# Kernel tuning notes

Hardware: AMD Instinct MI355X
Metric: run time of the kernel (lower is better)

## Reference

```python
import jax, jax.numpy as jnp
import numpy as np

D_MODEL = 1024
N_HEADS = 16
HEAD_DIM = D_MODEL // N_HEADS
D_FF = 4096
ROPE_BASE = 10000.0
LN_EPS = 1e-5


def setup_inputs() -> dict:
    key = jax.random.key(0)
    ks = jax.random.split(key, 12)
    B, S = 2, 2048
    s = 0.02
    inp = {
        "x": jax.random.normal(ks[0], (B, S, D_MODEL), dtype=jnp.float32),
        "Wq": jax.random.normal(ks[1], (D_MODEL, D_MODEL), dtype=jnp.float32) * s,
        "bq": jnp.zeros((D_MODEL,), jnp.float32),
        "Wk": jax.random.normal(ks[2], (D_MODEL, D_MODEL), dtype=jnp.float32) * s,
        "bk": jnp.zeros((D_MODEL,), jnp.float32),
        "Wv": jax.random.normal(ks[3], (D_MODEL, D_MODEL), dtype=jnp.float32) * s,
        "bv": jnp.zeros((D_MODEL,), jnp.float32),
        "Wo": jax.random.normal(ks[4], (D_MODEL, D_MODEL), dtype=jnp.float32) * s,
        "bo": jnp.zeros((D_MODEL,), jnp.float32),
        "ln1_g": jnp.ones((D_MODEL,), jnp.float32),
        "ln1_b": jnp.zeros((D_MODEL,), jnp.float32),
        "W1": jax.random.normal(ks[5], (D_MODEL, D_FF), dtype=jnp.float32) * s,
        "b1": jnp.zeros((D_FF,), jnp.float32),
        "W2": jax.random.normal(ks[6], (D_FF, D_MODEL), dtype=jnp.float32) * s,
        "b2": jnp.zeros((D_MODEL,), jnp.float32),
        "ln2_g": jnp.ones((D_MODEL,), jnp.float32),
        "ln2_b": jnp.zeros((D_MODEL,), jnp.float32),
    }
    return inp


def _layernorm(x, g, b):
    mu = jnp.mean(x, axis=-1, keepdims=True)
    var = jnp.var(x, axis=-1, keepdims=True)
    return (x - mu) * jax.lax.rsqrt(var + LN_EPS) * g + b


def _rope_cos_sin(seq_len, dtype):
    inv_freq = 1.0 / (ROPE_BASE ** (jnp.arange(0, HEAD_DIM, 2, dtype=jnp.float32) / HEAD_DIM))
    t = jnp.arange(seq_len, dtype=jnp.float32)
    freqs = jnp.einsum("i,j->ij", t, inv_freq)          # [S, HEAD_DIM/2]
    emb = jnp.concatenate([freqs, freqs], axis=-1)        # [S, HEAD_DIM]
    return jnp.cos(emb).astype(dtype), jnp.sin(emb).astype(dtype)


def _rotate_half(x):
    x1, x2 = jnp.split(x, 2, axis=-1)
    return jnp.concatenate([-x2, x1], axis=-1)


def reference(x, Wq, bq, Wk, bk, Wv, bv, Wo, bo, ln1_g, ln1_b,
              W1, b1, W2, b2, ln2_g, ln2_b):
    B, S, _ = x.shape
    residual = x
    h = _layernorm(x, ln1_g, ln1_b)

    def split_heads(y):  # [B,S,D] -> [B,H,S,hd]
        return y.reshape(B, S, N_HEADS, HEAD_DIM).transpose(0, 2, 1, 3)

    q = split_heads(h @ Wq + bq)
    k = split_heads(h @ Wk + bk)
    v = split_heads(h @ Wv + bv)

    cos, sin = _rope_cos_sin(S, x.dtype)  # [S, hd], broadcast over B,H
    q = q * cos + _rotate_half(q) * sin
    k = k * cos + _rotate_half(k) * sin

    scale = HEAD_DIM ** -0.5
    scores = jnp.einsum("bhqd,bhkd->bhqk", q, k) * scale
    attn = jax.nn.softmax(scores, axis=-1)
    ctx = jnp.einsum("bhqk,bhkd->bhqd", attn, v)           # [B,H,S,hd]
    ctx = ctx.transpose(0, 2, 1, 3).reshape(B, S, D_MODEL)
    attn_out = ctx @ Wo + bo

    x = residual + attn_out
    residual = x
    h = _layernorm(x, ln2_g, ln2_b)
    ffn = jax.nn.gelu(h @ W1 + b1, approximate=False) @ W2 + b2
    return residual + ffn
```

## Files before the change

kernel.cpp:

```cpp
#include <hip/hip_runtime.h>
#include <hip/hip_bf16.h>
#include <stdint.h>

#define S_LEN 2048
#define NH 16
#define HD 64
#define DM 1024
#define DFF 4096
#define MTOK 4096

typedef __attribute__((ext_vector_type(8))) short short8;
typedef __attribute__((ext_vector_type(4))) float f32x4;
typedef __attribute__((ext_vector_type(16))) float f32x16;
typedef __attribute__((ext_vector_type(2))) int i32x2;
typedef unsigned short u16;
typedef unsigned int u32;

__device__ __forceinline__ float bf2f(u16 u) {
  union { u32 i; float f; } x; x.i = ((u32)u) << 16; return x.f;
}
__device__ __forceinline__ u16 f2bf(float f) {
  union { float f; u32 i; } x; x.f = f;
  u32 r = x.i + 0x7fffu + ((x.i >> 16) & 1u);
  return (u16)(r >> 16);
}
__device__ __forceinline__ float exp2_fast(float x) {
  union { int i; float f; } u;
  u.i = (int)__builtin_fmaf(x, 8388608.0f, 1064986823.0f);
  return u.f;
}
__device__ __forceinline__ void gload16(const u16* g, u16* l) {
  __builtin_amdgcn_global_load_lds(
      (__attribute__((address_space(1))) u32*)g,
      (__attribute__((address_space(3))) u32*)l, 16, 0, 0);
}

#define VM0 asm volatile("s_waitcnt vmcnt(0)" ::: "memory")
#define VM6 asm volatile("s_waitcnt vmcnt(6)" ::: "memory")
#define BARR do { __builtin_amdgcn_s_barrier(); asm volatile("" ::: "memory"); } while (0)
#define LGKM0 do { asm volatile("s_waitcnt lgkmcnt(0)" ::: "memory"); __builtin_amdgcn_sched_barrier(0); } while (0)
#define PRIO1 __builtin_amdgcn_s_setprio(1)
#define PRIO0 __builtin_amdgcn_s_setprio(0)

__device__ __forceinline__ void transpose_tile(const float* __restrict__ W,
                                               u16* __restrict__ Wt, int K, int N,
                                               int n0, int k0, int tx, int ty,
                                               float (*tile)[33]) {
#pragma unroll
  for (int i = 0; i < 4; ++i)
    tile[ty + i * 8][tx] = W[(size_t)(k0 + ty + i * 8) * N + n0 + tx];
  __syncthreads();
#pragma unroll
  for (int i = 0; i < 4; ++i)
    Wt[(size_t)(n0 + ty + i * 8) * K + k0 + tx] = f2bf(tile[tx][ty + i * 8]);
}

__global__ __launch_bounds__(256) void prep(
    const float* __restrict__ Wq, const float* __restrict__ Wk,
    const float* __restrict__ Wv, const float* __restrict__ Wo,
    const float* __restrict__ W1, const float* __restrict__ W2,
    u16* __restrict__ WQKVT, u16* __restrict__ WOT, u16* __restrict__ W1T,
    u16* __restrict__ W2T, float* __restrict__ cosT, float* __restrict__ sinT,
    const float* __restrict__ x, const float* __restrict__ g,
    const float* __restrict__ b, u16* __restrict__ H) {
  __shared__ float tile[32][33];
  __shared__ float red[8];
  const int r = blockIdx.x;
  const int t = threadIdx.x;
  const int tx = t & 31, ty = t >> 5;
  if (r < 4096) {
    const float* W = (r < 1024) ? Wq : (r < 2048) ? Wk : (r < 3072) ? Wv : Wo;
    u16* Wt = (r < 1024) ? WQKVT
              : (r < 2048) ? WQKVT + 1024 * 1024
              : (r < 3072) ? WQKVT + 2 * 1024 * 1024 : WOT;
    int sub = r & 1023;
    transpose_tile(W, Wt, 1024, 1024, (sub & 31) * 32, (sub >> 5) * 32, tx, ty, tile);
  } else if (r < 8192) {
    int sub = r - 4096;
    transpose_tile(W1, W1T, 1024, 4096, (sub & 127) * 32, (sub >> 7) * 32, tx, ty, tile);
  } else if (r < 12288) {
    int sub = r - 8192;
    transpose_tile(W2, W2T, 4096, 1024, (sub & 31) * 32, (sub >> 5) * 32, tx, ty, tile);
  } else if (r < 12544) {
    int id = (r - 12288) * 256 + t;
    int s = id >> 5, j = id & 31;
    float inv = powf(10000.0f, -(float)j * (1.0f / 32.0f));
    float fr = (float)s * inv;
    cosT[id] = cosf(fr);
    sinT[id] = sinf(fr);
  } else {
    int row = r - 12544;
    float4 v = ((const float4*)(x + ((size_t)row << 10)))[t];
    float s = v.x + v.y + v.z + v.w;
    float q = v.x * v.x + v.y * v.y + v.z * v.z + v.w * v.w;
#pragma unroll
    for (int m = 1; m < 64; m <<= 1) {
      s += __shfl_xor(s, m, 64);
      q += __shfl_xor(q, m, 64);
    }
    int lane = t & 63, w = t >> 6;
    if (lane == 0) { red[w] = s; red[4 + w] = q; }
    __syncthreads();
    s = red[0] + red[1] + red[2] + red[3];
    q = red[4] + red[5] + red[6] + red[7];
    float mu = s * (1.0f / 1024.0f);
    float var = q * (1.0f / 1024.0f) - mu * mu;
    float rstd = rsqrtf(var + 1e-5f);
    float4 gv = ((const float4*)g)[t];
    float4 bv = ((const float4*)b)[t];
    ushort4 o;
    o.x = f2bf((v.x - mu) * rstd * gv.x + bv.x);
    o.y = f2bf((v.y - mu) * rstd * gv.y + bv.y);
    o.z = f2bf((v.z - mu) * rstd * gv.z + bv.z);
    o.w = f2bf((v.w - mu) * rstd * gv.w + bv.w);
    ((ushort4*)(H + ((size_t)row << 10)))[t] = o;
  }
}

__global__ __launch_bounds__(256) void ln_bf16(const float* __restrict__ x,
                                               const float* __restrict__ g,
                                               const float* __restrict__ b,
                                               u16* __restrict__ out) {
  int row = blockIdx.x;
  int t = threadIdx.x;
  float4 v = ((const float4*)(x + ((size_t)row << 10)))[t];
  float s = v.x + v.y + v.z + v.w;
  float q = v.x * v.x + v.y * v.y + v.z * v.z + v.w * v.w;
#pragma unroll
  for (int m = 1; m < 64; m <<= 1) {
    s += __shfl_xor(s, m, 64);
    q += __shfl_xor(q, m, 64);
  }
  __shared__ float red[8];
  int lane = t & 63, w = t >> 6;
  if (lane == 0) { red[w] = s; red[4 + w] = q; }
  __syncthreads();
  s = red[0] + red[1] + red[2] + red[3];
  q = red[4] + red[5] + red[6] + red[7];
  float mu = s * (1.0f / 1024.0f);
  float var = q * (1.0f / 1024.0f) - mu * mu;
  float rstd = rsqrtf(var + 1e-5f);
  float4 gv = ((const float4*)g)[t];
  float4 bv = ((const float4*)b)[t];
  ushort4 o;
  o.x = f2bf((v.x - mu) * rstd * gv.x + bv.x);
  o.y = f2bf((v.y - mu) * rstd * gv.y + bv.y);
  o.z = f2bf((v.z - mu) * rstd * gv.z + bv.z);
  o.w = f2bf((v.w - mu) * rstd * gv.w + bv.w);
  ((ushort4*)(out + ((size_t)row << 10)))[t] = o;
}

#define MMQ4(IB, NB)                                                         \
  _Pragma("unroll") for (int i_ = 0; i_ < 4; ++i_)                           \
  _Pragma("unroll") for (int n_ = 0; n_ < 2; ++n_)                           \
  _Pragma("unroll") for (int k_ = 0; k_ < 2; ++k_)                           \
    acc[(IB) + i_][(NB) + n_] = __builtin_amdgcn_mfma_f32_16x16x32_bf16(     \
        a[(IB) + i_][k_], b[(NB) + n_][k_], acc[(IB) + i_][(NB) + n_], 0, 0, 0);

template <int EPI>
__global__ __launch_bounds__(512, 1) void gemm256(
    const u16* __restrict__ A, const u16* __restrict__ Bt, int N, int K,
    const float* __restrict__ bias, const float* __restrict__ bq,
    const float* __restrict__ bk, const float* __restrict__ bv,
    const float* __restrict__ cosT, const float* __restrict__ sinT,
    u16* __restrict__ d0, u16* __restrict__ d1, u16* __restrict__ d2) {
  __shared__ __align__(16) u16 As[2][256 * 64];
  __shared__ __align__(16) u16 Bs[2][256 * 64];
  const int t = threadIdx.x;
  const int lane = t & 63, wid = t >> 6;
  const int fr = lane & 15, fq = lane >> 4;
  const int m0 = blockIdx.y << 8, n0 = blockIdx.x << 8;
  const int wmo = (wid >> 2) << 7;
  const int wno = (wid & 3) << 6;
  const int r7 = fr & 7;
  const int ssl = t & 7;
  const u16* Ap = A + (size_t)m0 * K;
  const u16* Bp = Bt + (size_t)n0 * K;

  f32x4 acc[8][4];
#pragma unroll
  for (int i = 0; i < 8; ++i)
#pragma unroll
    for (int n = 0; n < 4; ++n) acc[i][n] = (f32x4){0.f, 0.f, 0.f, 0.f};

  short8 a[8][2], b[4][2];

  auto stageH = [&](u16* dstSlot, const u16* src, int rowOff, int kt) {
#pragma unroll
    for (int c = 0; c < 2; ++c) {
      const int R = rowOff + (c << 6) + (t >> 3);
      gload16(src + (size_t)R * K + kt + ((ssl ^ (R & 7)) << 3),
              dstSlot + (size_t)R * 64 + ssl * 8);
    }
  };
  auto readAall = [&](int slot) {
#pragma unroll
    for (int i = 0; i < 8; ++i) {
      const u16* rp = &As[slot][(wmo + (i << 4) + fr) << 6];
      a[i][0] = *(const short8*)(rp + ((fq ^ r7) << 3));
      a[i][1] = *(const short8*)(rp + (((4 + fq) ^ r7) << 3));
    }
  };
  auto readB2 = [&](int slot, int nbase) {
#pragma unroll
    for (int n = 0; n < 2; ++n) {
      const u16* rp = &Bs[slot][(wno + ((nbase + n) << 4) + fr) << 6];
      b[nbase + n][0] = *(const short8*)(rp + ((fq ^ r7) << 3));
      b[nbase + n][1] = *(const short8*)(rp + (((4 + fq) ^ r7) << 3));
    }
  };

  const int nt = K >> 6;
  stageH(&As[0][0], Ap, 0, 0);
  stageH(&As[0][0], Ap, 128, 0);
  stageH(&Bs[0][0], Bp, 0, 0);
  stageH(&Bs[0][0], Bp, 128, 0);
  stageH(&As[1][0], Ap, 0, 64);
  stageH(&As[1][0], Ap, 128, 64);
  stageH(&Bs[1][0], Bp, 0, 64);

  for (int tt = 0; tt < nt; ++tt) {
    const int s = tt & 1;
    const int kt1 = (tt + 1) << 6, kt2 = (tt + 2) << 6;
    if (tt + 1 < nt) { VM6; } else { VM0; }
    BARR;
    readAall(s);
    readB2(s, 0);
    if (tt + 1 < nt) stageH(&Bs[s ^ 1][0], Bp, 128, kt1);
    LGKM0;
    PRIO1; MMQ4(0, 0); PRIO0;
    BARR;
    readB2(s, 2);
    if (tt + 2 < nt) stageH(&As[s][0], Ap, 0, kt2);
    LGKM0;
    PRIO1; MMQ4(0, 2); PRIO0;
    BARR;
    if (tt + 2 < nt) stageH(&As[s][0], Ap, 128, kt2);
    PRIO1; MMQ4(4, 2); PRIO0;
    BARR;
    if (tt + 2 < nt) stageH(&Bs[s][0], Bp, 0, kt2);
    PRIO1; MMQ4(4, 0); PRIO0;
  }

  if (EPI == 0) {
    const int colbase = n0 + wno;
    const int slice = colbase >> 10;
    const int cb = colbase & 1023;
    const int hh = cb >> 6;
    if (slice < 2) {
      const float sc = (slice == 0) ? 0.125f * 1.44269504088896f : 1.0f;
      const float* bb_ = (slice == 0) ? bq : bk;
      u16* dst = (slice == 0) ? d0 : d1;
#pragma unroll
      for (int i = 0; i < 8; ++i) {
        const int row0 = m0 + wmo + (i << 4) + (fq << 2);
#pragma unroll
        for (int n = 0; n < 2; ++n) {
          const int d = n * 16 + fr;
          const float blo = bb_[cb + d];
          const float bhi = bb_[cb + d + 32];
#pragma unroll
          for (int j = 0; j < 4; ++j) {
            const int row = row0 + j;
            const int ss = row & 2047, bb2 = row >> 11;
            const float c = cosT[ss * 32 + d];
            const float sn = sinT[ss * 32 + d];
            const float av = acc[i][n][j] + blo;
            const float bv2 = acc[i][n + 2][j] + bhi;
            const size_t base = ((size_t)((bb2 * 16 + hh) * 2048 + ss)) << 6;
            dst[base + d] = f2bf((av * c - bv2 * sn) * sc);
            dst[base + d + 32] = f2bf((bv2 * c + av * sn) * sc);
          }
        }
      }
    } else {
#pragma unroll
      for (int i = 0; i < 8; ++i) {
        const int row0 = m0 + wmo + (i << 4) + (fq << 2);
#pragma unroll
        for (int n = 0; n < 4; ++n) {
          const int d = n * 16 + fr;
          const float bia = bv[cb + d];
#pragma unroll
          for (int j = 0; j < 4; ++j) {
            const int row = row0 + j;
            const int ss = row & 2047, bb2 = row >> 11;
            d2[((size_t)((bb2 * 16 + hh) * 64 + d)) * 2048 + ss] =
                f2bf(acc[i][n][j] + bia);
          }
        }
      }
    }
  } else {
#pragma unroll
    for (int i = 0; i < 8; ++i) {
      const int row0 = m0 + wmo + (i << 4) + (fq << 2);
#pragma unroll
      for (int n = 0; n < 4; ++n) {
        const int col = n0 + wno + n * 16 + fr;
        const float bia = bias[col];
#pragma unroll
        for (int j = 0; j < 4; ++j) {
          const int row = row0 + j;
          const float v = acc[i][n][j] + bia;
          const float gl = 0.5f * v * (1.0f + erff(v * 0.70710678118f));
          d0[(size_t)row * N + col] = f2bf(gl);
        }
      }
    }
  }
}

__global__ __launch_bounds__(512, 1) void gemm_split(
    const u16* __restrict__ A, const u16* __restrict__ Bt, int K,
    const float* __restrict__ bias, const float* __restrict__ resid,
    float* __restrict__ dst) {
  __shared__ __align__(16) u16 As[2][128 * 128];
  __shared__ __align__(16) u16 Bs[2][128 * 128];
  const int t = threadIdx.x, lane = t & 63, w = t >> 6;
  const int fr = lane & 15, fq = lane >> 4;
  const int wq = w & 3, kh = w >> 2;
  const int wm = (wq >> 1) << 6, wn = (wq & 1) << 6;
  const int bid = blockIdx.x;
  const int xcd = bid & 7, within = bid >> 3;
  const int m0 = (xcd * 4 + (within >> 3)) << 7;
  const int n0 = (within & 7) << 7;
  const int srow = t >> 4;
  const int ssl = t & 15;

  f32x4 acc[4][4];
#pragma unroll
  for (int i = 0; i < 4; ++i)
#pragma unroll
    for (int n = 0; n < 4; ++n) acc[i][n] = (f32x4){0.f, 0.f, 0.f, 0.f};

  auto stage = [&](int buf, int kt) {
#pragma unroll
    for (int c = 0; c < 4; ++c) {
      const int R = c * 32 + srow;
      const int gs = ssl ^ (R & 15);
      gload16(A + (size_t)(m0 + R) * K + kt + gs * 8, &As[buf][R * 128 + ssl * 8]);
    }
#pragma unroll
    for (int c = 0; c < 4; ++c) {
      const int R = c * 32 + srow;
      const int gs = ssl ^ (R & 15);
      gload16(Bt + (size_t)(n0 + R) * K + kt + gs * 8, &Bs[buf][R * 128 + ssl * 8]);
    }
  };

  stage(0, 0);
  int buf = 0;
  const int iters = K >> 7;
  for (int it = 0; it < iters; ++it) {
    VM0;
    BARR;
    if (it + 1 < iters) stage(buf ^ 1, (it + 1) << 7);

    short8 a[4][2], b[4][2];
#pragma unroll
    for (int i = 0; i < 4; ++i) {
      const u16* rp = &As[buf][(wm + i * 16 + fr) * 128];
#pragma unroll
      for (int ks = 0; ks < 2; ++ks)
        a[i][ks] = *(const short8*)(rp + (((kh * 8 + ks * 4 + fq) ^ fr) << 3));
    }
#pragma unroll
    for (int n = 0; n < 4; ++n) {
      const u16* rp = &Bs[buf][(wn + n * 16 + fr) * 128];
#pragma unroll
      for (int ks = 0; ks < 2; ++ks)
        b[n][ks] = *(const short8*)(rp + (((kh * 8 + ks * 4 + fq) ^ fr) << 3));
    }
    PRIO1;
#pragma unroll
    for (int i = 0; i < 4; ++i)
#pragma unroll
      for (int n = 0; n < 4; ++n)
#pragma unroll
        for (int ks = 0; ks < 2; ++ks)
          acc[i][n] = __builtin_amdgcn_mfma_f32_16x16x32_bf16(a[i][ks], b[n][ks],
                                                              acc[i][n], 0, 0, 0);
    PRIO0;
    buf ^= 1;
  }

  BARR;
  float* mrg = (float*)&As[0][0];
  if (kh == 1) {
#pragma unroll
    for (int i = 0; i < 4; ++i) {
      const int ri = i * 16 + (fq << 2);
#pragma unroll
      for (int n = 0; n < 4; ++n) {
        const int ci = n * 16 + fr;
        *(f32x4*)(mrg + wq * 4352 + ci * 68 + ri) = acc[i][n];
      }
    }
  }
  LGKM0;
  BARR;
  if (kh == 0) {
#pragma unroll
    for (int i = 0; i < 4; ++i) {
      const int ri = i * 16 + (fq << 2);
      const int row0 = m0 + wm + ri;
#pragma unroll
      for (int n = 0; n < 4; ++n) {
        const int ci = n * 16 + fr;
        const int col = n0 + wn + ci;
        const f32x4 other = *(const f32x4*)(mrg + wq * 4352 + ci * 68 + ri);
        const float bia = bias[col];
#pragma unroll
        for (int j = 0; j < 4; ++j) {
          size_t idx = (size_t)(row0 + j) * 1024 + col;
          dst[idx] = acc[i][n][j] + other[j] + bia + resid[idx];
        }
      }
    }
  }
}

__global__ __launch_bounds__(512, 4) void attn_fwd(const u16* __restrict__ q,
                                                   const u16* __restrict__ k,
                                                   const u16* __restrict__ vt,
                                                   u16* __restrict__ ctx) {
  __shared__ __align__(16) u16 Ks[2][2][64 * 64];
  __shared__ __align__(16) u16 Vs[2][2][64 * 64];
  __shared__ float Lr[4][32];
  const int t = threadIdx.x, lane = t & 63, w = t >> 6;
  const int qsub = w & 3, half = w >> 2;
  const int ql = lane & 31;
  const int h = lane >> 5;
  const int bid = blockIdx.x;
  const int bh = (bid & 7) * 4 + ((bid >> 3) & 3);
  const int qt = bid >> 5;
  const int q0w = qt * 128 + qsub * 32;
  const size_t hbase = (size_t)bh << 17;
  const u16* kg = k + hbase;
  const u16* vg = vt + hbase;
  const int srow = t >> 3;
  const int sl = t & 7;
  const int l7 = lane & 7;

  short8 qf[4];
#pragma unroll
  for (int f = 0; f < 4; ++f)
    qf[f] = *(const short8*)(q + hbase + (size_t)(q0w + ql) * 64 + f * 16 + h * 8);

  float la[4] = {0.f, 0.f, 0.f, 0.f};
  f32x16 o[2];
#pragma unroll
  for (int db = 0; db < 2; ++db)
#pragma unroll
    for (int r = 0; r < 16; ++r) o[db][r] = 0.f;

  auto stage = [&](int buf, int it1) {
    const int kt0 = it1 << 6;
    const int kt1 = (16 + it1) << 6;
    const int gs = sl ^ (srow & 7);
    gload16(kg + (size_t)(kt0 + srow) * 64 + gs * 8, &Ks[0][buf][srow * 64 + sl * 8]);
    gload16(kg + (size_t)(kt1 + srow) * 64 + gs * 8, &Ks[1][buf][srow * 64 + sl * 8]);
    gload16(vg + (size_t)srow * 2048 + kt0 + gs * 8, &Vs[0][buf][srow * 64 + sl * 8]);
    gload16(vg + (size_t)srow * 2048 + kt1 + gs * 8, &Vs[1][buf][srow * 64 + sl * 8]);
  };

  stage(0, 0);
  int buf = 0;
  for (int it = 0; it < 16; ++it) {
    VM0;
    BARR;
    if (it < 15) stage(buf ^ 1, it + 1);

    f32x16 s[2];
    PRIO1;
#pragma unroll
    for (int kb = 0; kb < 2; ++kb) {
#pragma unroll
      for (int r = 0; r < 16; ++r) s[kb][r] = 0.f;
#pragma unroll
      for (int f = 0; f < 4; ++f) {
        const u16* kr = &Ks[half][buf][(kb * 32 + ql) * 64 + (((2 * f + h) ^ l7) << 3)];
        s[kb] = __builtin_amdgcn_mfma_f32_32x32x16_bf16(*(const short8*)kr, qf[f],
                                                        s[kb], 0, 0, 0);
      }
    }
    PRIO0;

    float p[2][16];
#pragma unroll
    for (int kb = 0; kb < 2; ++kb)
#pragma unroll
      for (int r = 0; r < 16; ++r) {
        p[kb][r] = exp2_fast(s[kb][r]);
        la[r & 3] += p[kb][r];
      }

    short8 pf[4];
#pragma unroll
    for (int kb = 0; kb < 2; ++kb)
#pragma unroll
      for (int rrp = 0; rrp < 2; ++rrp) {
        u32 y0, y1, x0, x1;
        asm volatile("v_cvt_pk_bf16_f32 %0, %1, %2" : "=v"(y0)
                     : "v"(p[kb][8 * rrp + 0]), "v"(p[kb][8 * rrp + 1]));
        asm volatile("v_cvt_pk_bf16_f32 %0, %1, %2" : "=v"(y1)
                     : "v"(p[kb][8 * rrp + 2]), "v"(p[kb][8 * rrp + 3]));
        asm volatile("v_cvt_pk_bf16_f32 %0, %1, %2" : "=v"(x0)
                     : "v"(p[kb][8 * rrp + 4]), "v"(p[kb][8 * rrp + 5]));
        asm volatile("v_cvt_pk_bf16_f32 %0, %1, %2" : "=v"(x1)
                     : "v"(p[kb][8 * rrp + 6]), "v"(p[kb][8 * rrp + 7]));
        i32x2 r0 = __builtin_amdgcn_permlane32_swap((int)x0, (int)y0, false, false);
        i32x2 r1 = __builtin_amdgcn_permlane32_swap((int)x1, (int)y1, false, false);
        u32 dw[4] = {(u32)r0[1], (u32)r1[1], (u32)r0[0], (u32)r1[0]};
        pf[kb * 2 + rrp] = *(short8*)dw;
      }

    PRIO1;
#pragma unroll
    for (int db = 0; db < 2; ++db) {
#pragma unroll
      for (int f = 0; f < 4; ++f) {
        const u16* vr = &Vs[half][buf][(db * 32 + ql) * 64 + (((2 * f + h) ^ l7) << 3)];
        o[db] = __builtin_amdgcn_mfma_f32_32x32x16_bf16(pf[f], *(const short8*)vr,
                                                        o[db], 0, 0, 0);
      }
    }
    PRIO0;
    buf ^= 1;
  }

  float lacc = (la[0] + la[1]) + (la[2] + la[3]);
  lacc += __shfl_xor(lacc, 32, 64);

  BARR;
  float* mO = (float*)&Ks[0][0][0];
  float* mL = (float*)&Vs[0][0][0];
  if (half == 1) {
#pragma unroll
    for (int r = 0; r < 16; ++r) {
      const int qr = (r & 3) + 8 * (r >> 2) + 4 * h;
#pragma unroll
      for (int db = 0; db < 2; ++db)
        mO[(qsub * 32 + qr) * 64 + db * 32 + ql] = o[db][r];
    }
    if (h == 0) mL[qsub * 32 + ql] = lacc;
  }
  LGKM0;
  BARR;
  if (half == 0) {
    float lsum = lacc + mL[qsub * 32 + ql];
    Lr[qsub][ql] = 1.0f / lsum;
#pragma unroll
    for (int r = 0; r < 16; ++r) {
      const int qr = (r & 3) + 8 * (r >> 2) + 4 * h;
#pragma unroll
      for (int db = 0; db < 2; ++db)
        o[db][r] += mO[(qsub * 32 + qr) * 64 + db * 32 + ql];
    }
    LGKM0;
    const int bb = bh >> 4, hh = bh & 15;
#pragma unroll
    for (int r = 0; r < 16; ++r) {
      const int qr = (r & 3) + 8 * (r >> 2) + 4 * h;
      const float rl = Lr[qsub][qr];
      const int row = q0w + qr;
      const size_t base = (((size_t)(bb * 2048 + row)) << 10) + hh * 64;
#pragma unroll
      for (int db = 0; db < 2; ++db)
        ctx[base + db * 32 + ql] = f2bf(o[db][r] * rl);
    }
  }
}

extern "C" void kernel_launch(void* const* d_in, const int* in_sizes, int n_in,
                              void* d_out, int out_size, void* d_ws, size_t ws_size,
                              hipStream_t stream) {
  const float* x    = (const float*)d_in[0];
  const float* Wq   = (const float*)d_in[1];
  const float* bq   = (const float*)d_in[2];
  const float* Wk   = (const float*)d_in[3];
  const float* bk   = (const float*)d_in[4];
  const float* Wv   = (const float*)d_in[5];
  const float* bv   = (const float*)d_in[6];
  const float* Wo   = (const float*)d_in[7];
  const float* bo   = (const float*)d_in[8];
  const float* ln1g = (const float*)d_in[9];
  const float* ln1b = (const float*)d_in[10];
  const float* W1   = (const float*)d_in[11];
  const float* b1   = (const float*)d_in[12];
  const float* W2   = (const float*)d_in[13];
  const float* b2   = (const float*)d_in[14];
  const float* ln2g = (const float*)d_in[15];
  const float* ln2b = (const float*)d_in[16];

  char* ws = (char*)d_ws;
  size_t off = 0;
  auto alloc = [&](size_t bytes) {
    char* p = ws + off;
    off += (bytes + 1023) & ~(size_t)1023;
    return p;
  };
  u16* WQKVT = (u16*)alloc((size_t)3 * DM * DM * 2);
  u16* WOT = (u16*)alloc((size_t)DM * DM * 2);
  u16* W1T = (u16*)alloc((size_t)DFF * DM * 2);
  u16* W2T = (u16*)alloc((size_t)DM * DFF * 2);
  float* COS = (float*)alloc((size_t)S_LEN * 32 * 4);
  float* SIN = (float*)alloc((size_t)S_LEN * 32 * 4);
  u16* H   = (u16*)alloc((size_t)MTOK * DM * 2);
  u16* Qb  = (u16*)alloc((size_t)MTOK * DM * 2);
  u16* Kb  = (u16*)alloc((size_t)MTOK * DM * 2);
  u16* VT  = (u16*)alloc((size_t)MTOK * DM * 2);
  u16* CTX = (u16*)alloc((size_t)MTOK * DM * 2);
  float* X2 = (float*)alloc((size_t)MTOK * DM * 4);
  u16* FFN1 = Qb;
  if (ws_size < off) return;

  dim3 blk256(256);
  prep<<<dim3(16640), blk256, 0, stream>>>(Wq, Wk, Wv, Wo, W1, W2, WQKVT, WOT,
                                           W1T, W2T, COS, SIN, x, ln1g, ln1b, H);
  gemm256<0><<<dim3(12, 16), dim3(512), 0, stream>>>(
      H, WQKVT, 3072, 1024, nullptr, bq, bk, bv, COS, SIN, Qb, Kb, VT);
  attn_fwd<<<dim3(512), dim3(512), 0, stream>>>(Qb, Kb, VT, CTX);
  gemm_split<<<dim3(256), dim3(512), 0, stream>>>(CTX, WOT, 1024, bo, x, X2);
  ln_bf16<<<4096, blk256, 0, stream>>>(X2, ln2g, ln2b, H);
  gemm256<1><<<dim3(16, 16), dim3(512), 0, stream>>>(
      H, W1T, 4096, 1024, b1, nullptr, nullptr, nullptr, nullptr, nullptr,
      FFN1, nullptr, nullptr);
  gemm_split<<<dim3(256), dim3(512), 0, stream>>>(FFN1, W2T, 4096, b2, X2, (float*)d_out);
}
```

Measured before the change: 220.2 us.

## Halve A-fragment registers and re-split GEMM staging into quarter-tile loads

The 256x256 GEMM mainloop now keeps only four A fragments in registers instead of eight, reading the two halves of the A tile in separate phases. Global-to-LDS staging is split into 64-row quarter loads that are reordered so each LDS region is refilled only after its last read. The vmcnt wait and barrier move to the end of each iteration. The aim is to cut VGPR pressure and spread loads more evenly, at the cost of extra barriers and LDS reads per k-step.

After: 223.6 us. Within noise of the previous version (+1.6%).

```diff
diff --git a/kernel.cpp b/kernel.cpp
--- a/kernel.cpp
+++ b/kernel.cpp
@@ -155,7 +155,7 @@
   _Pragma("unroll") for (int n_ = 0; n_ < 2; ++n_)                           \
   _Pragma("unroll") for (int k_ = 0; k_ < 2; ++k_)                           \
     acc[(IB) + i_][(NB) + n_] = __builtin_amdgcn_mfma_f32_16x16x32_bf16(     \
-        a[(IB) + i_][k_], b[(NB) + n_][k_], acc[(IB) + i_][(NB) + n_], 0, 0, 0);
+        a[i_][k_], b[(NB) + n_][k_], acc[(IB) + i_][(NB) + n_], 0, 0, 0);
 
 template <int EPI>
 __global__ __launch_bounds__(512, 1) void gemm256(
@@ -183,20 +183,17 @@
 #pragma unroll
     for (int n = 0; n < 4; ++n) acc[i][n] = (f32x4){0.f, 0.f, 0.f, 0.f};
 
-  short8 a[8][2], b[4][2];
-
-  auto stageH = [&](u16* dstSlot, const u16* src, int rowOff, int kt) {
-#pragma unroll
-    for (int c = 0; c < 2; ++c) {
-      const int R = rowOff + (c << 6) + (t >> 3);
-      gload16(src + (size_t)R * K + kt + ((ssl ^ (R & 7)) << 3),
-              dstSlot + (size_t)R * 64 + ssl * 8);
-    }
+  short8 a[4][2], b[4][2];
+
+  auto stageQ = [&](u16* dstSlot, const u16* src, int rowOff, int kt) {
+    const int R = rowOff + (t >> 3);
+    gload16(src + (size_t)R * K + kt + ((ssl ^ (R & 7)) << 3),
+            dstSlot + (size_t)R * 64 + ssl * 8);
   };
-  auto readAall = [&](int slot) {
-#pragma unroll
-    for (int i = 0; i < 8; ++i) {
-      const u16* rp = &As[slot][(wmo + (i << 4) + fr) << 6];
+  auto readA4 = [&](int slot, int ibase) {
+#pragma unroll
+    for (int i = 0; i < 4; ++i) {
+      const u16* rp = &As[slot][(wmo + ((ibase + i) << 4) + fr) << 6];
       a[i][0] = *(const short8*)(rp + ((fq ^ r7) << 3));
       a[i][1] = *(const short8*)(rp + (((4 + fq) ^ r7) << 3));
     }
@@ -211,35 +208,43 @@
   };
 
   const int nt = K >> 6;
-  stageH(&As[0][0], Ap, 0, 0);
-  stageH(&As[0][0], Ap, 128, 0);
-  stageH(&Bs[0][0], Bp, 0, 0);
-  stageH(&Bs[0][0], Bp, 128, 0);
-  stageH(&As[1][0], Ap, 0, 64);
-  stageH(&As[1][0], Ap, 128, 64);
-  stageH(&Bs[1][0], Bp, 0, 64);
+  stageQ(&As[0][0], Ap, 0, 0);   stageQ(&As[0][0], Ap, 64, 0);
+  stageQ(&As[0][0], Ap, 128, 0); stageQ(&As[0][0], Ap, 192, 0);
+  stageQ(&Bs[0][0], Bp, 0, 0);   stageQ(&Bs[0][0], Bp, 64, 0);
+  stageQ(&Bs[0][0], Bp, 128, 0); stageQ(&Bs[0][0], Bp, 192, 0);
+  stageQ(&As[1][0], Ap, 0, 64);  stageQ(&As[1][0], Ap, 128, 64);
+  stageQ(&Bs[1][0], Bp, 0, 64);  stageQ(&Bs[1][0], Bp, 64, 64);
+  stageQ(&As[1][0], Ap, 64, 64); stageQ(&As[1][0], Ap, 192, 64);
+  if (nt > 1) { VM6; } else { VM0; }
+  BARR;
 
   for (int tt = 0; tt < nt; ++tt) {
     const int s = tt & 1;
+    u16* Asl = &As[s][0];
+    u16* Bsl = &Bs[s][0];
+    u16* Bnx = &Bs[s ^ 1][0];
     const int kt1 = (tt + 1) << 6, kt2 = (tt + 2) << 6;
-    if (tt + 1 < nt) { VM6; } else { VM0; }
-    BARR;
-    readAall(s);
-    readB2(s, 0);
-    if (tt + 1 < nt) stageH(&Bs[s ^ 1][0], Bp, 128, kt1);
-    LGKM0;
+    const bool st1 = (tt + 1 < nt), st2 = (tt + 2 < nt);
+    readA4(s, 0); readB2(s, 0);
+    if (st1) { stageQ(Bnx, Bp, 128, kt1); stageQ(Bnx, Bp, 192, kt1); }
+    BARR; LGKM0;
     PRIO1; MMQ4(0, 0); PRIO0;
     BARR;
     readB2(s, 2);
-    if (tt + 2 < nt) stageH(&As[s][0], Ap, 0, kt2);
-    LGKM0;
+    if (st2) { stageQ(Asl, Ap, 0, kt2); stageQ(Asl, Ap, 128, kt2); }
+    BARR; LGKM0;
     PRIO1; MMQ4(0, 2); PRIO0;
     BARR;
-    if (tt + 2 < nt) stageH(&As[s][0], Ap, 128, kt2);
+    readA4(s, 4);
+    if (st2) { stageQ(Bsl, Bp, 0, kt2); stageQ(Bsl, Bp, 64, kt2); }
+    BARR; LGKM0;
     PRIO1; MMQ4(4, 2); PRIO0;
     BARR;
-    if (tt + 2 < nt) stageH(&Bs[s][0], Bp, 0, kt2);
+    if (st2) { stageQ(Asl, Ap, 64, kt2); stageQ(Asl, Ap, 192, kt2); }
+    BARR;
     PRIO1; MMQ4(4, 0); PRIO0;
+    if (st2) { VM6; } else { VM0; }
+    BARR;
   }
 
   if (EPI == 0) {
```
